# Performance work log

Measured on AMD Instinct MI355X. Metric: run time of the kernel, lower is better.

## Reference

```python
import jax, jax.numpy as jnp
import numpy as np

N = 50000
E = 800000
IN, HID, OUT = 256, 128, 64
BN_EPS = 1e-5

def sage(x, src, dst, Wl, bl, Wr):
    # PyG SAGEConv (aggr='mean'): lin_l(mean_j x_j) + lin_r(x_root)
    agg = jax.ops.segment_sum(x[src], dst, num_segments=N)
    deg = jax.ops.segment_sum(jnp.ones((src.shape[0], 1), x.dtype), dst, num_segments=N)
    mean_agg = agg / jnp.maximum(deg, 1.0)
    return mean_agg @ Wl + bl + x @ Wr

def bn_eval(x, gamma, beta):
    # eval-mode BatchNorm1d with running_mean=0, running_var=1
    return x * (gamma / jnp.sqrt(1.0 + BN_EPS)) + beta

def setup_inputs() -> dict:
    key = jax.random.key(0)
    ks = jax.random.split(key, 16)
    g = lambda k, shp, s: jax.random.normal(k, shp, jnp.float32) * s
    inp = {
        'x': g(ks[0], (N, IN), 1.0),
        'edge_index': jax.random.randint(ks[1], (2, E), 0, N, jnp.int32),
        'eps': g(ks[2], (10, N, OUT), 1.0),
        'W1l': g(ks[3], (IN, HID), 0.06), 'b1': jnp.zeros((HID,), jnp.float32), 'W1r': g(ks[4], (IN, HID), 0.06),
        'g1': jnp.ones((HID,), jnp.float32), 'be1': jnp.zeros((HID,), jnp.float32),
        'W2l': g(ks[5], (HID, 2 * HID), 0.09), 'b2': jnp.zeros((2 * HID,), jnp.float32), 'W2r': g(ks[6], (HID, 2 * HID), 0.09),
        'g2': jnp.ones((2 * HID,), jnp.float32), 'be2': jnp.zeros((2 * HID,), jnp.float32),
        'W3l': g(ks[7], (2 * HID, 2 * OUT), 0.06), 'b3': jnp.zeros((2 * OUT,), jnp.float32), 'W3r': g(ks[8], (2 * HID, 2 * OUT), 0.06),
        'Wd1': g(ks[9], (OUT, HID), 0.12), 'bd1': jnp.zeros((HID,), jnp.float32),
        'g3': jnp.ones((HID,), jnp.float32), 'be3': jnp.zeros((HID,), jnp.float32),
        'Wd2': g(ks[10], (HID, IN), 0.09), 'bd2': jnp.zeros((IN,), jnp.float32),
    }
    return inp

def reference(x, edge_index, eps, W1l, b1, W1r, g1, be1, W2l, b2, W2r, g2, be2,
              W3l, b3, W3r, Wd1, bd1, g3, be3, Wd2, bd2):
    src, dst = edge_index[0], edge_index[1]
    # encode (dropout is identity in eval mode)
    x1 = bn_eval(jax.nn.relu(sage(x, src, dst, W1l, b1, W1r)), g1, be1)
    x2 = bn_eval(jax.nn.relu(sage(x1, src, dst, W2l, b2, W2r)), g2, be2)
    mz = sage(x2, src, dst, W3l, b3, W3r)
    mean, log_std = mz[:, :OUT], mz[:, OUT:]
    # reparameterize: average of n_samples draws == mean + std * mean(eps)
    std = jnp.exp(log_std)
    z = mean + std * jnp.mean(eps, axis=0)
    # decode
    h = bn_eval(jax.nn.relu(z @ Wd1 + bd1), g3, be3) + x1
    return h @ Wd2 + bd2
```

## Files before the change

### kernel.cpp

```cpp
#include <hip/hip_runtime.h>


typedef unsigned short u16;
typedef short bf16x8 __attribute__((ext_vector_type(8)));
typedef float f32x4  __attribute__((ext_vector_type(4)));

constexpr float BN_EPS = 1e-5f;

__device__ __forceinline__ u16 f2bf(float f) {
    unsigned u = __float_as_uint(f);
    return (u16)((u + 0x7FFFu + ((u >> 16) & 1u)) >> 16);
}
__device__ __forceinline__ float bf2f(u16 h) {
    return __uint_as_float(((unsigned)h) << 16);
}
__device__ __forceinline__ void gl_lds16(const void* g, void* l) {
    __builtin_amdgcn_global_load_lds(
        (const __attribute__((address_space(1))) unsigned*)g,
        (__attribute__((address_space(3))) unsigned*)l, 16, 0, 0);
}


__global__ void hist_kernel(const int* __restrict__ dst, int E, int* __restrict__ deg) {
    int e = blockIdx.x * 256 + threadIdx.x;
    if (e < E) atomicAdd(&deg[dst[e]], 1);
}

__global__ __launch_bounds__(256)
void scan_partial(const int* __restrict__ deg, int N, int* __restrict__ bsum) {
    __shared__ int sd[256];
    int i = blockIdx.x * 256 + threadIdx.x;
    int v = (i < N) ? deg[i] : 0;
    sd[threadIdx.x] = v;
    __syncthreads();
    for (int off = 128; off > 0; off >>= 1) {
        if (threadIdx.x < off) sd[threadIdx.x] += sd[threadIdx.x + off];
        __syncthreads();
    }
    if (threadIdx.x == 0) bsum[blockIdx.x] = sd[0];
}

__global__ __launch_bounds__(1024)
void scan_bsum(int* __restrict__ bsum, int nb) {
    __shared__ int sd[1024];
    int t = threadIdx.x;
    int v = (t < nb) ? bsum[t] : 0;
    sd[t] = v;
    __syncthreads();
    for (int off = 1; off < 1024; off <<= 1) {
        int u = (t >= off) ? sd[t - off] : 0;
        __syncthreads();
        sd[t] += u;
        __syncthreads();
    }
    if (t < nb) bsum[t] = sd[t] - v;
}

__global__ __launch_bounds__(256)
void scan_final(const int* __restrict__ deg, const int* __restrict__ bsum, int N, int E,
                int* __restrict__ row_ptr, int* __restrict__ cursor,
                float* __restrict__ inv_deg) {
    __shared__ int sd[256];
    int i = blockIdx.x * 256 + threadIdx.x;
    int d = (i < N) ? deg[i] : 0;
    sd[threadIdx.x] = d;
    __syncthreads();
    for (int off = 1; off < 256; off <<= 1) {
        int u = (threadIdx.x >= off) ? sd[threadIdx.x - off] : 0;
        __syncthreads();
        sd[threadIdx.x] += u;
        __syncthreads();
    }
    if (i < N) {
        int excl = bsum[blockIdx.x] + sd[threadIdx.x] - d;
        row_ptr[i] = excl;
        cursor[i]  = excl;
        inv_deg[i] = 1.0f / (float)max(d, 1);
        if (i == N - 1) row_ptr[N] = E;
    }
}

__global__ void fill_kernel(const int* __restrict__ src, const int* __restrict__ dst,
                            int E, int* __restrict__ cursor, int* __restrict__ csr) {
    int e = blockIdx.x * 256 + threadIdx.x;
    if (e < E) {
        int p = atomicAdd(&cursor[dst[e]], 1);
        csr[p] = src[e];
    }
}


__global__ void pack_all(const float* __restrict__ W1l, const float* __restrict__ W1r,
                         const float* __restrict__ W2l, const float* __restrict__ W2r,
                         const float* __restrict__ W3l, const float* __restrict__ W3r,
                         const float* __restrict__ Wd1, const float* __restrict__ Wd2,
                         u16* __restrict__ Bt1, u16* __restrict__ Bt2,
                         u16* __restrict__ Bt3, u16* __restrict__ Btd1,
                         u16* __restrict__ Btd2) {
    int idx = blockIdx.x * 256 + threadIdx.x;
    if (idx < 65536) {
        int c = idx >> 8, k = idx & 255;
        float v = (c < 128) ? W1l[k * 128 + c] : W1r[k * 128 + (c - 128)];
        Bt1[c * 256 + k] = f2bf(v);
    } else if (idx < 131072) {
        int i2 = idx - 65536;
        int c = i2 >> 8, k = i2 & 255;
        float v = (k < 128) ? W2l[k * 256 + c] : W2r[(k - 128) * 256 + c];
        Bt2[c * 256 + k] = f2bf(v);
    } else if (idx < 196608) {
        int i2 = idx - 131072;
        int c = i2 >> 8, k = i2 & 255;
        float v = (c < 128) ? W3l[k * 128 + c] : W3r[k * 128 + (c - 128)];
        Bt3[c * 256 + k] = f2bf(v);
    } else if (idx < 204800) {
        int i2 = idx - 196608;
        int c = i2 >> 6, k = i2 & 63;
        Btd1[i2] = f2bf(Wd1[k * 128 + c]);
    } else if (idx < 237568) {
        int i2 = idx - 204800;
        int c = i2 >> 7, k = i2 & 127;
        Btd2[i2] = f2bf(Wd2[k * 256 + c]);
    }
}


__global__ void cast_x(const float* __restrict__ x, u16* __restrict__ xb, int N, int Mpad) {
    int idx = blockIdx.x * 256 + threadIdx.x;
    if (idx >= Mpad * 64) return;
    int row = idx >> 6, q = idx & 63;
    float4 v = make_float4(0.f, 0.f, 0.f, 0.f);
    if (row < N) v = *(const float4*)&x[(size_t)row * 256 + q * 4];
    ushort4 o;
    o.x = f2bf(v.x); o.y = f2bf(v.y); o.z = f2bf(v.z); o.w = f2bf(v.w);
    *(ushort4*)&xb[(size_t)row * 256 + q * 4] = o;
}


template<int K, int NC, int EPI, bool F32OUT>
__global__ __launch_bounds__(256)
void mgemm(const u16* __restrict__ A, const u16* __restrict__ Bt,
           const float* __restrict__ bias, const float* __restrict__ gamma,
           const float* __restrict__ beta,
           const u16* __restrict__ skip, int skip_ld,
           void* __restrict__ Cout, int M) {
    __shared__ char lds[32768];
    char* As0 = lds;
    char* As1 = lds + 8192;
    char* Bs0 = lds + 16384;
    char* Bs1 = lds + 24576;

    const int t = threadIdx.x;
    const int l = t & 63;
    const int wave = t >> 6;
    const int wr = wave >> 1, wc = wave & 1;
    const int lr = l & 15, kg = l >> 4;
    const int row0 = blockIdx.x * 128;
    const int col0 = blockIdx.y * 128;

    f32x4 acc[4][4];
    #pragma unroll
    for (int m = 0; m < 4; m++)
        #pragma unroll
        for (int n = 0; n < 4; n++)
            #pragma unroll
            for (int r = 0; r < 4; r++) acc[m][n][r] = 0.f;

    const u16* Ab = A  + (size_t)row0 * K;
    const u16* Bb = Bt + (size_t)col0 * K;

    const int sr  = t >> 2;
    const int sq  = (t & 3) ^ ((t >> 3) & 3);
    auto stage = [&](const u16* g, char* lb, int k0) {
        gl_lds16(g + (size_t)sr * K + k0 + sq * 8,        lb + wave * 1024);
        gl_lds16(g + (size_t)(sr + 64) * K + k0 + sq * 8, lb + 4096 + wave * 1024);
    };

    stage(Ab, As0, 0);
    stage(Bb, Bs0, 0);
    __syncthreads();

    const int swz = (kg ^ ((lr >> 1) & 3)) << 4;
    constexpr int NT = K / 32;
    for (int ks = 0; ks < NT; ks++) {
        char* Ac = (ks & 1) ? As1 : As0;
        char* Bc = (ks & 1) ? Bs1 : Bs0;
        if (ks + 1 < NT) {
            char* An = (ks & 1) ? As0 : As1;
            char* Bn = (ks & 1) ? Bs0 : Bs1;
            stage(Ab, An, (ks + 1) * 32);
            stage(Bb, Bn, (ks + 1) * 32);
        }
        bf16x8 af[4], bfr[4];
        #pragma unroll
        for (int m = 0; m < 4; m++)
            af[m] = *(const bf16x8*)(Ac + wr * 4096 + m * 1024 + lr * 64 + swz);
        #pragma unroll
        for (int n = 0; n < 4; n++)
            bfr[n] = *(const bf16x8*)(Bc + wc * 4096 + n * 1024 + lr * 64 + swz);
        #pragma unroll
        for (int m = 0; m < 4; m++)
            #pragma unroll
            for (int n = 0; n < 4; n++)
                acc[m][n] = __builtin_amdgcn_mfma_f32_16x16x32_bf16(
                    af[m], bfr[n], acc[m][n], 0, 0, 0);
        __syncthreads();
    }

    const float rs = rsqrtf(1.0f + BN_EPS);
    const int colb = col0 + wc * 64;
    const int rowb = row0 + wr * 64;
    float bia[4], gpr[4], bet[4];
    if (EPI == 1 || EPI == 2) {
        #pragma unroll
        for (int n = 0; n < 4; n++) {
            int c = colb + n * 16 + lr;
            bia[n] = bias[c];
            gpr[n] = gamma[c] * rs;
            bet[n] = beta[c];
        }
    } else if (EPI == 3) {
        #pragma unroll
        for (int n = 0; n < 4; n++) bia[n] = bias[colb + n * 16 + lr];
    }
    __syncthreads();

    char* rp = lds + wave * 4096;
    #pragma unroll
    for (int m = 0; m < 4; m++) {
        #pragma unroll
        for (int n = 0; n < 4; n++) {
            #pragma unroll
            for (int r = 0; r < 4; r++) {
                float v = acc[m][n][r];
                if (EPI == 1 || EPI == 2) {
                    v += bia[n];
                    v = fmaxf(v, 0.f);
                    v = v * gpr[n] + bet[n];
                }
                if (EPI == 2)
                    v += bf2f(skip[(size_t)(rowb + m * 16 + kg * 4 + r) * skip_ld
                                   + colb + n * 16 + lr]);
                if (EPI == 3) v += bia[n];
                int rl = kg * 4 + r, cl = n * 16 + lr;
                if (F32OUT) ((float*)rp)[rl * 64 + cl] = v;
                else        ((u16*)rp)[rl * 64 + cl]   = f2bf(v);
            }
        }
        if (F32OUT) {
            float* rpf = (float*)rp;
            #pragma unroll
            for (int rr = 0; rr < 4; rr++) {
                int rloc = rr * 4 + kg;
                int grow = rowb + m * 16 + rloc;
                if (grow < M) {
                    f32x4 v4 = *(f32x4*)&rpf[rloc * 64 + lr * 4];
                    *(f32x4*)((float*)Cout + (size_t)grow * NC + colb + lr * 4) = v4;
                }
            }
        } else {
            u16* rph = (u16*)rp;
            #pragma unroll
            for (int hh = 0; hh < 2; hh++) {
                int rloc = hh * 8 + (l >> 3);
                int grow = rowb + m * 16 + rloc;
                bf16x8 v8 = *(bf16x8*)&rph[rloc * 64 + (l & 7) * 8];
                *(bf16x8*)((u16*)Cout + (size_t)grow * NC + colb + (l & 7) * 8) = v8;
            }
        }
    }
}


__global__ __launch_bounds__(256)
void agg1_kernel(const u16* __restrict__ Y1, const int* __restrict__ row_ptr,
                 const int* __restrict__ csr, const float* __restrict__ inv_deg,
                 const float* __restrict__ b1, const float* __restrict__ g1,
                 const float* __restrict__ be1, u16* __restrict__ catX, int N) {
    int g   = (blockIdx.x * 256 + threadIdx.x) >> 4;
    int sub = threadIdx.x & 15;
    if (g >= N) return;
    int b = row_ptr[g], e = row_ptr[g + 1];
    const int off = sub * 8;
    float a[8] = {};
    int ee = b;
    for (; ee + 1 < e; ee += 2) {
        int j0 = csr[ee], j1 = csr[ee + 1];
        bf16x8 v0 = *(const bf16x8*)&Y1[(size_t)j0 * 256 + off];
        bf16x8 v1 = *(const bf16x8*)&Y1[(size_t)j1 * 256 + off];
        #pragma unroll
        for (int r = 0; r < 8; r++)
            a[r] += bf2f((u16)v0[r]) + bf2f((u16)v1[r]);
    }
    if (ee < e) {
        bf16x8 v0 = *(const bf16x8*)&Y1[(size_t)csr[ee] * 256 + off];
        #pragma unroll
        for (int r = 0; r < 8; r++) a[r] += bf2f((u16)v0[r]);
    }
    float id = inv_deg[g];
    bf16x8 u = *(const bf16x8*)&Y1[(size_t)g * 256 + 128 + off];
    const float rs = rsqrtf(1.0f + BN_EPS);
    bf16x8 o;
    #pragma unroll
    for (int r = 0; r < 8; r++) {
        int c = off + r;
        float v = a[r] * id + b1[c] + bf2f((u16)u[r]);
        v = fmaxf(v, 0.f);
        v = v * (g1[c] * rs) + be1[c];
        o[r] = (short)f2bf(v);
    }
    *(bf16x8*)&catX[(size_t)g * 256 + 128 + off] = o;
}

__global__ __launch_bounds__(256)
void agg2_kernel(const int* __restrict__ row_ptr, const int* __restrict__ csr,
                 const float* __restrict__ inv_deg, u16* __restrict__ catX, int N) {
    int g   = (blockIdx.x * 256 + threadIdx.x) >> 4;
    int sub = threadIdx.x & 15;
    if (g >= N) return;
    int b = row_ptr[g], e = row_ptr[g + 1];
    const int off = sub * 8;
    float a[8] = {};
    int ee = b;
    for (; ee + 1 < e; ee += 2) {
        int j0 = csr[ee], j1 = csr[ee + 1];
        bf16x8 v0 = *(const bf16x8*)&catX[(size_t)j0 * 256 + 128 + off];
        bf16x8 v1 = *(const bf16x8*)&catX[(size_t)j1 * 256 + 128 + off];
        #pragma unroll
        for (int r = 0; r < 8; r++)
            a[r] += bf2f((u16)v0[r]) + bf2f((u16)v1[r]);
    }
    if (ee < e) {
        bf16x8 v0 = *(const bf16x8*)&catX[(size_t)csr[ee] * 256 + 128 + off];
        #pragma unroll
        for (int r = 0; r < 8; r++) a[r] += bf2f((u16)v0[r]);
    }
    float id = inv_deg[g];
    bf16x8 o;
    #pragma unroll
    for (int r = 0; r < 8; r++) o[r] = (short)f2bf(a[r] * id);
    *(bf16x8*)&catX[(size_t)g * 256 + off] = o;
}

__global__ __launch_bounds__(256)
void agg3_kernel(const u16* __restrict__ Y3, const int* __restrict__ row_ptr,
                 const int* __restrict__ csr, const float* __restrict__ inv_deg,
                 const float* __restrict__ b3, const float* __restrict__ eps,
                 u16* __restrict__ z, int N) {
    int g   = (blockIdx.x * 256 + threadIdx.x) >> 4;
    int sub = threadIdx.x & 15;
    if (g >= N) return;
    int b = row_ptr[g], e = row_ptr[g + 1];
    const int off = sub * 8;

    f32x4 emv = {0.f, 0.f, 0.f, 0.f};
    #pragma unroll
    for (int t10 = 0; t10 < 10; t10++) {
        f32x4 v = *(const f32x4*)&eps[((size_t)t10 * N + g) * 64 + sub * 4];
        emv += v;
    }
    emv *= 0.1f;

    float a[8] = {};
    int ee = b;
    for (; ee + 1 < e; ee += 2) {
        int j0 = csr[ee], j1 = csr[ee + 1];
        bf16x8 v0 = *(const bf16x8*)&Y3[(size_t)j0 * 256 + off];
        bf16x8 v1 = *(const bf16x8*)&Y3[(size_t)j1 * 256 + off];
        #pragma unroll
        for (int r = 0; r < 8; r++)
            a[r] += bf2f((u16)v0[r]) + bf2f((u16)v1[r]);
    }
    if (ee < e) {
        bf16x8 v0 = *(const bf16x8*)&Y3[(size_t)csr[ee] * 256 + off];
        #pragma unroll
        for (int r = 0; r < 8; r++) a[r] += bf2f((u16)v0[r]);
    }
    float id = inv_deg[g];
    bf16x8 u = *(const bf16x8*)&Y3[(size_t)g * 256 + 128 + off];
    float mzv[8];
    #pragma unroll
    for (int r = 0; r < 8; r++)
        mzv[r] = a[r] * id + b3[off + r] + bf2f((u16)u[r]);

    const int wl = threadIdx.x & 63;
    const int wb = wl & ~15;
    const int s0 = wb + ((2 * sub) & 15);
    const int s1 = wb + ((2 * sub + 1) & 15);
    float em8[8];
    #pragma unroll
    for (int q = 0; q < 4; q++) {
        em8[q]     = __shfl(emv[q], s0);
        em8[4 + q] = __shfl(emv[q], s1);
    }
    float hi[8];
    #pragma unroll
    for (int r = 0; r < 8; r++) hi[r] = __shfl_xor(mzv[r], 8);

    if (sub < 8) {
        bf16x8 o;
        #pragma unroll
        for (int r = 0; r < 8; r++)
            o[r] = (short)f2bf(mzv[r] + expf(hi[r]) * em8[r]);
        *(bf16x8*)&z[(size_t)g * 64 + sub * 8] = o;
    }
}


extern "C" void kernel_launch(void* const* d_in, const int* in_sizes, int n_in,
                              void* d_out, int out_size, void* d_ws, size_t ws_size,
                              hipStream_t stream) {
    const float* x    = (const float*)d_in[0];
    const int*   ei   = (const int*)d_in[1];
    const float* eps  = (const float*)d_in[2];
    const float* W1l  = (const float*)d_in[3];
    const float* b1   = (const float*)d_in[4];
    const float* W1r  = (const float*)d_in[5];
    const float* g1   = (const float*)d_in[6];
    const float* be1  = (const float*)d_in[7];
    const float* W2l  = (const float*)d_in[8];
    const float* b2   = (const float*)d_in[9];
    const float* W2r  = (const float*)d_in[10];
    const float* g2   = (const float*)d_in[11];
    const float* be2  = (const float*)d_in[12];
    const float* W3l  = (const float*)d_in[13];
    const float* b3   = (const float*)d_in[14];
    const float* W3r  = (const float*)d_in[15];
    const float* Wd1  = (const float*)d_in[16];
    const float* bd1  = (const float*)d_in[17];
    const float* g3   = (const float*)d_in[18];
    const float* be3  = (const float*)d_in[19];
    const float* Wd2  = (const float*)d_in[20];
    const float* bd2  = (const float*)d_in[21];

    const int Nn   = in_sizes[0] / 256;
    const int E    = in_sizes[1] / 2;
    const int Mpad = ((Nn + 127) / 128) * 128;
    const int* srcp = ei;
    const int* dstp = ei + E;
    const int nb = (Nn + 255) / 256;

    char* w = (char*)d_ws;
    auto alloc = [&](size_t bytes) -> void* {
        void* p = (void*)w;
        w += (bytes + 255) & ~(size_t)255;
        return p;
    };
    int*   deg     = (int*)  alloc((size_t)Nn * 4);
    int*   bsum    = (int*)  alloc((size_t)nb * 4);
    int*   row_ptr = (int*)  alloc((size_t)(Nn + 1) * 4);
    int*   cursor  = (int*)  alloc((size_t)Nn * 4);
    float* inv_deg = (float*)alloc((size_t)Nn * 4);
    int*   csr     = (int*)  alloc((size_t)E * 4);
    u16*   Bt1     = (u16*)  alloc(256 * 256 * 2);
    u16*   Bt2     = (u16*)  alloc(256 * 256 * 2);
    u16*   Bt3     = (u16*)  alloc(256 * 256 * 2);
    u16*   Btd1    = (u16*)  alloc(128 * 64 * 2);
    u16*   Btd2    = (u16*)  alloc(256 * 128 * 2);
    u16*   xb      = (u16*)  alloc((size_t)Mpad * 256 * 2);
    u16*   zb      = (u16*)  alloc((size_t)Mpad * 64 * 2);
    u16*   bufA    = (u16*)  alloc((size_t)Mpad * 256 * 2);
    u16*   bufB    = (u16*)  alloc((size_t)Mpad * 256 * 2);
    u16*   bufC    = (u16*)  alloc((size_t)Mpad * 256 * 2);
    if ((size_t)(w - (char*)d_ws) > ws_size) return;

    hipMemsetAsync(deg, 0, (size_t)Nn * 4, stream);
    hist_kernel<<<(E + 255) / 256, 256, 0, stream>>>(dstp, E, deg);
    scan_partial<<<nb, 256, 0, stream>>>(deg, Nn, bsum);
    scan_bsum<<<1, 1024, 0, stream>>>(bsum, nb);
    scan_final<<<nb, 256, 0, stream>>>(deg, bsum, Nn, E, row_ptr, cursor, inv_deg);
    fill_kernel<<<(E + 255) / 256, 256, 0, stream>>>(srcp, dstp, E, cursor, csr);

    pack_all<<<(237568 + 255) / 256, 256, 0, stream>>>(
        W1l, W1r, W2l, W2r, W3l, W3r, Wd1, Wd2, Bt1, Bt2, Bt3, Btd1, Btd2);
    cast_x<<<(Mpad * 64 + 255) / 256, 256, 0, stream>>>(x, xb, Nn, Mpad);

    dim3 g2c(Mpad / 128, 2);
    dim3 g1c(Mpad / 128, 1);
    const int aggBlocks = (Nn + 15) / 16;

    mgemm<256, 256, 0, false><<<g2c, 256, 0, stream>>>(
        xb, Bt1, nullptr, nullptr, nullptr, nullptr, 0, bufA, Mpad);
    agg1_kernel<<<aggBlocks, 256, 0, stream>>>(bufA, row_ptr, csr, inv_deg,
                                               b1, g1, be1, bufB, Nn);
    agg2_kernel<<<aggBlocks, 256, 0, stream>>>(row_ptr, csr, inv_deg, bufB, Nn);
    mgemm<256, 256, 1, false><<<g2c, 256, 0, stream>>>(
        bufB, Bt2, b2, g2, be2, nullptr, 0, bufA, Mpad);
    mgemm<256, 256, 0, false><<<g2c, 256, 0, stream>>>(
        bufA, Bt3, nullptr, nullptr, nullptr, nullptr, 0, bufC, Mpad);
    agg3_kernel<<<aggBlocks, 256, 0, stream>>>(bufC, row_ptr, csr, inv_deg,
                                               b3, eps, zb, Nn);
    mgemm<64, 128, 2, false><<<g1c, 256, 0, stream>>>(
        zb, Btd1, bd1, g3, be3,  bufB + 128, 256, bufC, Mpad);
    mgemm<128, 256, 3, true><<<g2c, 256, 0, stream>>>(
        bufC, Btd2, bd2, nullptr, nullptr, nullptr, 0, d_out, Nn);
}
```

Baseline: 319.1 us.

## Fuse decoder GEMMs, merge scan and cast kernels, unroll aggregation loops

The two decoder GEMMs become one kernel that keeps the hidden activation (ReLU, BN and skip add) in LDS as bf16, so the intermediate no longer round-trips through global memory and one launch disappears. The block-sum scan is folded into the final scan kernel, with each block summing its predecessors' partials, and weight packing is merged with the x cast, removing two more launches. The neighbour-aggregation loops are unrolled to four edges per iteration to put more gathers in flight. In exchange the fused decoder uses 64KB of LDS, which limits occupancy, and writes its output through per-wave LDS staging.

After: 302.7 us. 1.05x faster.

```diff
diff --git a/kernel.cpp b/kernel.cpp
--- a/kernel.cpp
+++ b/kernel.cpp
@@ -18,6 +18,15 @@
     __builtin_amdgcn_global_load_lds(
         (const __attribute__((address_space(1))) unsigned*)g,
         (__attribute__((address_space(3))) unsigned*)l, 16, 0, 0);
+}
+
+template<int KS>
+__device__ __forceinline__ void stage_panel(const u16* g, char* lb, int k0, int t) {
+    const int sr   = t >> 2;
+    const int sq   = (t & 3) ^ ((t >> 3) & 3);
+    const int wave = t >> 6;
+    gl_lds16(g + (size_t)sr * KS + k0 + sq * 8,        lb + wave * 1024);
+    gl_lds16(g + (size_t)(sr + 64) * KS + k0 + sq * 8, lb + 4096 + wave * 1024);
 }
 
 
@@ -40,39 +49,34 @@
     if (threadIdx.x == 0) bsum[blockIdx.x] = sd[0];
 }
 
-__global__ __launch_bounds__(1024)
-void scan_bsum(int* __restrict__ bsum, int nb) {
-    __shared__ int sd[1024];
+__global__ __launch_bounds__(256)
+void scan_final2(const int* __restrict__ deg, const int* __restrict__ bsum,
+                 int N, int E, int* __restrict__ row_ptr, int* __restrict__ cursor,
+                 float* __restrict__ inv_deg) {
+    __shared__ int sd[256];
     int t = threadIdx.x;
-    int v = (t < nb) ? bsum[t] : 0;
-    sd[t] = v;
-    __syncthreads();
-    for (int off = 1; off < 1024; off <<= 1) {
+    int partial = 0;
+    for (int j = t; j < blockIdx.x; j += 256) partial += bsum[j];
+    sd[t] = partial;
+    __syncthreads();
+    for (int off = 128; off > 0; off >>= 1) {
+        if (t < off) sd[t] += sd[t + off];
+        __syncthreads();
+    }
+    int base = sd[0];
+    __syncthreads();
+    int i = blockIdx.x * 256 + t;
+    int d = (i < N) ? deg[i] : 0;
+    sd[t] = d;
+    __syncthreads();
+    for (int off = 1; off < 256; off <<= 1) {
         int u = (t >= off) ? sd[t - off] : 0;
         __syncthreads();
         sd[t] += u;
         __syncthreads();
     }
-    if (t < nb) bsum[t] = sd[t] - v;
-}
-
-__global__ __launch_bounds__(256)
-void scan_final(const int* __restrict__ deg, const int* __restrict__ bsum, int N, int E,
-                int* __restrict__ row_ptr, int* __restrict__ cursor,
-                float* __restrict__ inv_deg) {
-    __shared__ int sd[256];
-    int i = blockIdx.x * 256 + threadIdx.x;
-    int d = (i < N) ? deg[i] : 0;
-    sd[threadIdx.x] = d;
-    __syncthreads();
-    for (int off = 1; off < 256; off <<= 1) {
-        int u = (threadIdx.x >= off) ? sd[threadIdx.x - off] : 0;
-        __syncthreads();
-        sd[threadIdx.x] += u;
-        __syncthreads();
-    }
     if (i < N) {
-        int excl = bsum[blockIdx.x] + sd[threadIdx.x] - d;
+        int excl = base + sd[t] - d;
         row_ptr[i] = excl;
         cursor[i]  = excl;
         inv_deg[i] = 1.0f / (float)max(d, 1);
@@ -90,13 +94,15 @@
 }
 
 
-__global__ void pack_all(const float* __restrict__ W1l, const float* __restrict__ W1r,
-                         const float* __restrict__ W2l, const float* __restrict__ W2r,
-                         const float* __restrict__ W3l, const float* __restrict__ W3r,
-                         const float* __restrict__ Wd1, const float* __restrict__ Wd2,
-                         u16* __restrict__ Bt1, u16* __restrict__ Bt2,
-                         u16* __restrict__ Bt3, u16* __restrict__ Btd1,
-                         u16* __restrict__ Btd2) {
+__global__ void pack_cast(const float* __restrict__ x,
+                          const float* __restrict__ W1l, const float* __restrict__ W1r,
+                          const float* __restrict__ W2l, const float* __restrict__ W2r,
+                          const float* __restrict__ W3l, const float* __restrict__ W3r,
+                          const float* __restrict__ Wd1, const float* __restrict__ Wd2,
+                          u16* __restrict__ Bt1, u16* __restrict__ Bt2,
+                          u16* __restrict__ Bt3, u16* __restrict__ Btd1,
+                          u16* __restrict__ Btd2, u16* __restrict__ xb,
+                          int N, int Mpad) {
     int idx = blockIdx.x * 256 + threadIdx.x;
     if (idx < 65536) {
         int c = idx >> 8, k = idx & 255;
@@ -121,18 +127,14 @@
         int c = i2 >> 7, k = i2 & 127;
         Btd2[i2] = f2bf(Wd2[k * 256 + c]);
     }
-}
-
-
-__global__ void cast_x(const float* __restrict__ x, u16* __restrict__ xb, int N, int Mpad) {
-    int idx = blockIdx.x * 256 + threadIdx.x;
-    if (idx >= Mpad * 64) return;
-    int row = idx >> 6, q = idx & 63;
-    float4 v = make_float4(0.f, 0.f, 0.f, 0.f);
-    if (row < N) v = *(const float4*)&x[(size_t)row * 256 + q * 4];
-    ushort4 o;
-    o.x = f2bf(v.x); o.y = f2bf(v.y); o.z = f2bf(v.z); o.w = f2bf(v.w);
-    *(ushort4*)&xb[(size_t)row * 256 + q * 4] = o;
+    if (idx < Mpad * 64) {
+        int row = idx >> 6, q = idx & 63;
+        float4 v = make_float4(0.f, 0.f, 0.f, 0.f);
+        if (row < N) v = *(const float4*)&x[(size_t)row * 256 + q * 4];
+        ushort4 o;
+        o.x = f2bf(v.x); o.y = f2bf(v.y); o.z = f2bf(v.z); o.w = f2bf(v.w);
+        *(ushort4*)&xb[(size_t)row * 256 + q * 4] = o;
+    }
 }
 
 
@@ -168,15 +170,8 @@
     const u16* Ab = A  + (size_t)row0 * K;
     const u16* Bb = Bt + (size_t)col0 * K;
 
-    const int sr  = t >> 2;
-    const int sq  = (t & 3) ^ ((t >> 3) & 3);
-    auto stage = [&](const u16* g, char* lb, int k0) {
-        gl_lds16(g + (size_t)sr * K + k0 + sq * 8,        lb + wave * 1024);
-        gl_lds16(g + (size_t)(sr + 64) * K + k0 + sq * 8, lb + 4096 + wave * 1024);
-    };
-
-    stage(Ab, As0, 0);
-    stage(Bb, Bs0, 0);
+    stage_panel<K>(Ab, As0, 0, t);
+    stage_panel<K>(Bb, Bs0, 0, t);
     __syncthreads();
 
     const int swz = (kg ^ ((lr >> 1) & 3)) << 4;
@@ -185,10 +180,8 @@
         char* Ac = (ks & 1) ? As1 : As0;
         char* Bc = (ks & 1) ? Bs1 : Bs0;
         if (ks + 1 < NT) {
-            char* An = (ks & 1) ? As0 : As1;
-            char* Bn = (ks & 1) ? Bs0 : Bs1;
-            stage(Ab, An, (ks + 1) * 32);
-            stage(Bb, Bn, (ks + 1) * 32);
+            stage_panel<K>(Ab, (ks & 1) ? As0 : As1, (ks + 1) * 32, t);
+            stage_panel<K>(Bb, (ks & 1) ? Bs0 : Bs1, (ks + 1) * 32, t);
         }
         bf16x8 af[4], bfr[4];
         #pragma unroll
@@ -272,6 +265,145 @@
 
 
 __global__ __launch_bounds__(256)
+void dec_fused(const u16* __restrict__ zb, const u16* __restrict__ Btd1,
+               const u16* __restrict__ Btd2, const float* __restrict__ bd1,
+               const float* __restrict__ g3, const float* __restrict__ be3,
+               const u16* __restrict__ x1, const float* __restrict__ bd2,
+               float* __restrict__ out, int M) {
+    __shared__ char lds[65536];
+    const int t = threadIdx.x;
+    const int l = t & 63;
+    const int wave = t >> 6;
+    const int wr = wave >> 1, wc = wave & 1;
+    const int lr = l & 15, kg = l >> 4;
+    const int row0 = blockIdx.x * 128;
+    const float rs = rsqrtf(1.0f + BN_EPS);
+    const int swz = (kg ^ ((lr >> 1) & 3)) << 4;
+    char* hb = lds + 32768;
+
+    stage_panel<64>(zb + (size_t)row0 * 64, lds,         0, t);
+    stage_panel<64>(zb + (size_t)row0 * 64, lds + 8192, 32, t);
+    stage_panel<64>(Btd1, lds + 16384,  0, t);
+    stage_panel<64>(Btd1, lds + 24576, 32, t);
+    __syncthreads();
+
+    f32x4 acc[4][4];
+    #pragma unroll
+    for (int m = 0; m < 4; m++)
+        #pragma unroll
+        for (int n = 0; n < 4; n++)
+            #pragma unroll
+            for (int r = 0; r < 4; r++) acc[m][n][r] = 0.f;
+
+    #pragma unroll
+    for (int ks = 0; ks < 2; ks++) {
+        char* Ac = lds + ks * 8192;
+        char* Bc = lds + 16384 + ks * 8192;
+        bf16x8 af[4], bfr[4];
+        #pragma unroll
+        for (int m = 0; m < 4; m++)
+            af[m] = *(const bf16x8*)(Ac + wr * 4096 + m * 1024 + lr * 64 + swz);
+        #pragma unroll
+        for (int n = 0; n < 4; n++)
+            bfr[n] = *(const bf16x8*)(Bc + wc * 4096 + n * 1024 + lr * 64 + swz);
+        #pragma unroll
+        for (int m = 0; m < 4; m++)
+            #pragma unroll
+            for (int n = 0; n < 4; n++)
+                acc[m][n] = __builtin_amdgcn_mfma_f32_16x16x32_bf16(
+                    af[m], bfr[n], acc[m][n], 0, 0, 0);
+    }
+
+    {
+        float bia[4], gpr[4], bet[4];
+        #pragma unroll
+        for (int n = 0; n < 4; n++) {
+            int c = wc * 64 + n * 16 + lr;
+            bia[n] = bd1[c];
+            gpr[n] = g3[c] * rs;
+            bet[n] = be3[c];
+        }
+        #pragma unroll
+        for (int m = 0; m < 4; m++)
+            #pragma unroll
+            for (int n = 0; n < 4; n++)
+                #pragma unroll
+                for (int r = 0; r < 4; r++) {
+                    int rl = wr * 64 + m * 16 + kg * 4 + r;
+                    int cl = wc * 64 + n * 16 + lr;
+                    float v = acc[m][n][r] + bia[n];
+                    v = fmaxf(v, 0.f) * gpr[n] + bet[n];
+                    v += bf2f(x1[(size_t)(row0 + rl) * 256 + cl]);
+                    int slot = (cl >> 3) ^ (rl & 7);
+                    ((u16*)(hb + rl * 256 + slot * 16))[cl & 7] = f2bf(v);
+                }
+    }
+    __syncthreads();
+
+    for (int ch = 0; ch < 2; ch++) {
+        const u16* Bb2 = Btd2 + ch * 16384;
+        stage_panel<128>(Bb2, lds, 0, t);
+        #pragma unroll
+        for (int m = 0; m < 4; m++)
+            #pragma unroll
+            for (int n = 0; n < 4; n++)
+                #pragma unroll
+                for (int r = 0; r < 4; r++) acc[m][n][r] = 0.f;
+        __syncthreads();
+
+        for (int ks = 0; ks < 4; ks++) {
+            char* Bc = lds + (ks & 1) * 8192;
+            if (ks + 1 < 4)
+                stage_panel<128>(Bb2, lds + (((ks & 1) ^ 1) * 8192), (ks + 1) * 32, t);
+            bf16x8 af[4], bfr[4];
+            #pragma unroll
+            for (int m = 0; m < 4; m++) {
+                int row = wr * 64 + m * 16 + lr;
+                int s = (ks * 4 + kg) ^ (row & 7);
+                af[m] = *(const bf16x8*)(hb + row * 256 + s * 16);
+            }
+            #pragma unroll
+            for (int n = 0; n < 4; n++)
+                bfr[n] = *(const bf16x8*)(Bc + wc * 4096 + n * 1024 + lr * 64 + swz);
+            #pragma unroll
+            for (int m = 0; m < 4; m++)
+                #pragma unroll
+                for (int n = 0; n < 4; n++)
+                    acc[m][n] = __builtin_amdgcn_mfma_f32_16x16x32_bf16(
+                        af[m], bfr[n], acc[m][n], 0, 0, 0);
+            __syncthreads();
+        }
+
+        const int colb = ch * 128 + wc * 64;
+        const int rowb = row0 + wr * 64;
+        float b2v[4];
+        #pragma unroll
+        for (int n = 0; n < 4; n++) b2v[n] = bd2[colb + n * 16 + lr];
+        char* rp = lds + wave * 4096;
+        #pragma unroll
+        for (int m = 0; m < 4; m++) {
+            #pragma unroll
+            for (int n = 0; n < 4; n++)
+                #pragma unroll
+                for (int r = 0; r < 4; r++)
+                    ((float*)rp)[(kg * 4 + r) * 64 + n * 16 + lr] = acc[m][n][r] + b2v[n];
+            float* rpf = (float*)rp;
+            #pragma unroll
+            for (int rr = 0; rr < 4; rr++) {
+                int rloc = rr * 4 + kg;
+                int grow = rowb + m * 16 + rloc;
+                if (grow < M) {
+                    f32x4 v4 = *(f32x4*)&rpf[rloc * 64 + lr * 4];
+                    *(f32x4*)&out[(size_t)grow * 256 + colb + lr * 4] = v4;
+                }
+            }
+        }
+        __syncthreads();
+    }
+}
+
+
+__global__ __launch_bounds__(256)
 void agg1_kernel(const u16* __restrict__ Y1, const int* __restrict__ row_ptr,
                  const int* __restrict__ csr, const float* __restrict__ inv_deg,
                  const float* __restrict__ b1, const float* __restrict__ g1,
@@ -283,15 +415,18 @@
     const int off = sub * 8;
     float a[8] = {};
     int ee = b;
-    for (; ee + 1 < e; ee += 2) {
-        int j0 = csr[ee], j1 = csr[ee + 1];
+    for (; ee + 3 < e; ee += 4) {
+        int j0 = csr[ee], j1 = csr[ee + 1], j2 = csr[ee + 2], j3 = csr[ee + 3];
         bf16x8 v0 = *(const bf16x8*)&Y1[(size_t)j0 * 256 + off];
         bf16x8 v1 = *(const bf16x8*)&Y1[(size_t)j1 * 256 + off];
+        bf16x8 v2 = *(const bf16x8*)&Y1[(size_t)j2 * 256 + off];
+        bf16x8 v3 = *(const bf16x8*)&Y1[(size_t)j3 * 256 + off];
         #pragma unroll
         for (int r = 0; r < 8; r++)
-            a[r] += bf2f((u16)v0[r]) + bf2f((u16)v1[r]);
-    }
-    if (ee < e) {
+            a[r] += (bf2f((u16)v0[r]) + bf2f((u16)v1[r]))
+                  + (bf2f((u16)v2[r]) + bf2f((u16)v3[r]));
+    }
+    for (; ee < e; ee++) {
         bf16x8 v0 = *(const bf16x8*)&Y1[(size_t)csr[ee] * 256 + off];
         #pragma unroll
         for (int r = 0; r < 8; r++) a[r] += bf2f((u16)v0[r]);
@@ -321,15 +456,18 @@
     const int off = sub * 8;
     float a[8] = {};
     int ee = b;
-    for (; ee + 1 < e; ee += 2) {
-        int j0 = csr[ee], j1 = csr[ee + 1];
+    for (; ee + 3 < e; ee += 4) {
+        int j0 = csr[ee], j1 = csr[ee + 1], j2 = csr[ee + 2], j3 = csr[ee + 3];
         bf16x8 v0 = *(const bf16x8*)&catX[(size_t)j0 * 256 + 128 + off];
         bf16x8 v1 = *(const bf16x8*)&catX[(size_t)j1 * 256 + 128 + off];
+        bf16x8 v2 = *(const bf16x8*)&catX[(size_t)j2 * 256 + 128 + off];
+        bf16x8 v3 = *(const bf16x8*)&catX[(size_t)j3 * 256 + 128 + off];
         #pragma unroll
         for (int r = 0; r < 8; r++)
-            a[r] += bf2f((u16)v0[r]) + bf2f((u16)v1[r]);
-    }
-    if (ee < e) {
+            a[r] += (bf2f((u16)v0[r]) + bf2f((u16)v1[r]))
+                  + (bf2f((u16)v2[r]) + bf2f((u16)v3[r]));
+    }
+    for (; ee < e; ee++) {
         bf16x8 v0 = *(const bf16x8*)&catX[(size_t)csr[ee] * 256 + 128 + off];
         #pragma unroll
         for (int r = 0; r < 8; r++) a[r] += bf2f((u16)v0[r]);
@@ -362,15 +500,18 @@
 
     float a[8] = {};
     int ee = b;
-    for (; ee + 1 < e; ee += 2) {
-        int j0 = csr[ee], j1 = csr[ee + 1];
+    for (; ee + 3 < e; ee += 4) {
+        int j0 = csr[ee], j1 = csr[ee + 1], j2 = csr[ee + 2], j3 = csr[ee + 3];
         bf16x8 v0 = *(const bf16x8*)&Y3[(size_t)j0 * 256 + off];
         bf16x8 v1 = *(const bf16x8*)&Y3[(size_t)j1 * 256 + off];
+        bf16x8 v2 = *(const bf16x8*)&Y3[(size_t)j2 * 256 + off];
+        bf16x8 v3 = *(const bf16x8*)&Y3[(size_t)j3 * 256 + off];
         #pragma unroll
         for (int r = 0; r < 8; r++)
-            a[r] += bf2f((u16)v0[r]) + bf2f((u16)v1[r]);
-    }
-    if (ee < e) {
+            a[r] += (bf2f((u16)v0[r]) + bf2f((u16)v1[r]))
+                  + (bf2f((u16)v2[r]) + bf2f((u16)v3[r]));
+    }
+    for (; ee < e; ee++) {
         bf16x8 v0 = *(const bf16x8*)&Y3[(size_t)csr[ee] * 256 + off];
         #pragma unroll
         for (int r = 0; r < 8; r++) a[r] += bf2f((u16)v0[r]);
@@ -466,16 +607,14 @@
     hipMemsetAsync(deg, 0, (size_t)Nn * 4, stream);
     hist_kernel<<<(E + 255) / 256, 256, 0, stream>>>(dstp, E, deg);
     scan_partial<<<nb, 256, 0, stream>>>(deg, Nn, bsum);
-    scan_bsum<<<1, 1024, 0, stream>>>(bsum, nb);
-    scan_final<<<nb, 256, 0, stream>>>(deg, bsum, Nn, E, row_ptr, cursor, inv_deg);
+    scan_final2<<<nb, 256, 0, stream>>>(deg, bsum, Nn, E, row_ptr, cursor, inv_deg);
     fill_kernel<<<(E + 255) / 256, 256, 0, stream>>>(srcp, dstp, E, cursor, csr);
 
-    pack_all<<<(237568 + 255) / 256, 256, 0, stream>>>(
-        W1l, W1r, W2l, W2r, W3l, W3r, Wd1, Wd2, Bt1, Bt2, Bt3, Btd1, Btd2);
-    cast_x<<<(Mpad * 64 + 255) / 256, 256, 0, stream>>>(x, xb, Nn, Mpad);
+    pack_cast<<<(Mpad * 64 + 255) / 256, 256, 0, stream>>>(
+        x, W1l, W1r, W2l, W2r, W3l, W3r, Wd1, Wd2,
+        Bt1, Bt2, Bt3, Btd1, Btd2, xb, Nn, Mpad);
 
     dim3 g2c(Mpad / 128, 2);
-    dim3 g1c(Mpad / 128, 1);
     const int aggBlocks = (Nn + 15) / 16;
 
     mgemm<256, 256, 0, false><<<g2c, 256, 0, stream>>>(
@@ -489,8 +628,6 @@
         bufA, Bt3, nullptr, nullptr, nullptr, nullptr, 0, bufC, Mpad);
     agg3_kernel<<<aggBlocks, 256, 0, stream>>>(bufC, row_ptr, csr, inv_deg,
                                                b3, eps, zb, Nn);
-    mgemm<64, 128, 2, false><<<g1c, 256, 0, stream>>>(
-        zb, Btd1, bd1, g3, be3,  bufB + 128, 256, bufC, Mpad);
-    mgemm<128, 256, 3, true><<<g2c, 256, 0, stream>>>(
-        bufC, Btd2, bd2, nullptr, nullptr, nullptr, 0, d_out, Nn);
-}
+    dec_fused<<<Mpad / 128, 256, 0, stream>>>(
+        zb, Btd1, Btd2, bd1, g3, be3, bufB + 128, bd2, (float*)d_out, Nn);
+}
```
